# Performance work log

Measured on AMD Instinct MI355X. Metric: run time of the kernel, lower is better.

## Reference

```python
import itertools
import jax, jax.numpy as jnp
import numpy as np

# ---- JPEG constants (match utils.y_table / utils.c_table) ----
_Y_TABLE = np.array([
    [16, 11, 10, 16, 24, 40, 51, 61],
    [12, 12, 14, 19, 26, 58, 60, 55],
    [14, 13, 16, 24, 40, 57, 69, 56],
    [14, 17, 22, 29, 51, 87, 80, 62],
    [18, 22, 37, 56, 68, 109, 103, 77],
    [24, 35, 55, 64, 81, 104, 113, 92],
    [49, 64, 78, 87, 103, 121, 120, 101],
    [72, 92, 95, 98, 112, 100, 103, 99]], dtype=np.float32)
_C_TABLE = np.full((8, 8), 99, dtype=np.float32)
_C_TABLE[:4, :4] = np.array([[17, 18, 24, 47], [18, 21, 26, 66],
                             [24, 26, 56, 99], [47, 66, 99, 99]], dtype=np.float32)

# RGB -> YCbCr matrix (code defines M then uses M.T via tensordot dims=1)
_YCBCR_M = np.array([[0.299, 0.587, 0.114],
                     [-0.168736, -0.331264, 0.5],
                     [0.5, -0.418688, -0.081312]], dtype=np.float32)
_SHIFT = np.array([0.0, 128.0, 128.0], dtype=np.float32)

_cx = np.cos((2 * np.arange(8)[:, None] + 1) * np.arange(8)[None, :] * np.pi / 16)  # [x,u]
_DCT = np.einsum('xu,yv->xyuv', _cx, _cx).astype(np.float32)
_alpha = np.array([1.0 / np.sqrt(2)] + [1.0] * 7)
_DCT_SCALE = (np.outer(_alpha, _alpha) * 0.25).astype(np.float32)

FACTOR = 1.0
K = 8  # block size


def _block_split(x):
    # x: [B, H, W] -> [B, H*W/64, 8, 8]
    B, H, W = x.shape
    x = x.reshape(B, H // K, K, W // K, K)
    x = jnp.transpose(x, (0, 1, 3, 2, 4))
    return x.reshape(B, -1, K, K)


def _dct_8x8(x):
    # x: [B, N, 8, 8]
    x = x - 128.0
    return jnp.asarray(_DCT_SCALE) * jnp.einsum('bnxy,xyuv->bnuv', x, jnp.asarray(_DCT))


def _avg_pool2(x):
    # 2x2 average pooling, stride 2; x: [B, H, W]
    B, H, W = x.shape
    return x.reshape(B, H // 2, 2, W // 2, 2).mean(axis=(2, 4))


def _compress(image):
    # image: [B, 3, H, W] in [0, 1]
    img = jnp.transpose(image * 255.0, (0, 2, 3, 1))  # [B, H, W, 3]
    ycbcr = jnp.einsum('bhwc,cd->bhwd', img, jnp.asarray(_YCBCR_M.T)) + jnp.asarray(_SHIFT)
    y = ycbcr[..., 0]
    cb = _avg_pool2(ycbcr[..., 1])
    cr = _avg_pool2(ycbcr[..., 2])
    y_q = jnp.round(_dct_8x8(_block_split(y)) / (jnp.asarray(_Y_TABLE) * FACTOR))
    cb_q = jnp.round(_dct_8x8(_block_split(cb)) / (jnp.asarray(_C_TABLE) * FACTOR))
    cr_q = jnp.round(_dct_8x8(_block_split(cr)) / (jnp.asarray(_C_TABLE) * FACTOR))
    return y_q, cb_q, cr_q


def setup_inputs() -> dict:
    key = jax.random.key(0)
    image = jax.random.uniform(key, (32, 3, 512, 512), dtype=jnp.float32)
    return {"image": image}


def reference(image):
    return _compress(image)
```

## Files before the change

kernel.cpp:

```cpp
#include <hip/hip_runtime.h>
#include <cmath>


namespace jc {

constexpr double c1 = 0.98078528040323044912618223613424;
constexpr double c2 = 0.92387953251128675612818318939679;
constexpr double c3 = 0.83146961230254523707878837761791;
constexpr double c4 = 0.70710678118654752440084436210485;
constexpr double c5 = 0.55557023301960222474283081394853;
constexpr double c6 = 0.38268343236508977172845998403040;
constexpr double c7 = 0.19509032201612826784828486847702;
constexpr double alpha0 = 0.70710678118654746171979706919384;

struct Tab {
  float t[4096];
  float sc[64];
  float yq[64];
  float cq[64];
  constexpr Tab() : t(), sc(), yq(), cq() {
    const double CX[8][8] = {
      {1.0,  c1,  c2,  c3,  c4,  c5,  c6,  c7},
      {1.0,  c3,  c6, -c7, -c4, -c1, -c2, -c5},
      {1.0,  c5, -c6, -c1, -c4,  c7,  c2,  c3},
      {1.0,  c7, -c2, -c5,  c4,  c3, -c6, -c1},
      {1.0, -c7, -c2,  c5,  c4, -c3, -c6,  c1},
      {1.0, -c5, -c6,  c1, -c4, -c7,  c2, -c3},
      {1.0, -c3,  c6,  c7, -c4,  c1, -c2,  c5},
      {1.0, -c1,  c2, -c3,  c4, -c5,  c6, -c7}};
    for (int i = 0; i < 64; ++i) {
      const int u = i >> 3, v = i & 7;
      for (int j = 0; j < 64; ++j) {
        const int x = j >> 3, y = j & 7;
        t[i * 64 + j] = (float)(CX[x][u] * CX[y][v]);
      }
      const double au = (u == 0) ? alpha0 : 1.0;
      const double av = (v == 0) ? alpha0 : 1.0;
      sc[i] = (float)((au * av) * 0.25);
    }
    const int YT[64] = {
      16, 11, 10, 16, 24, 40, 51, 61,
      12, 12, 14, 19, 26, 58, 60, 55,
      14, 13, 16, 24, 40, 57, 69, 56,
      14, 17, 22, 29, 51, 87, 80, 62,
      18, 22, 37, 56, 68, 109, 103, 77,
      24, 35, 55, 64, 81, 104, 113, 92,
      49, 64, 78, 87, 103, 121, 120, 101,
      72, 92, 95, 98, 112, 100, 103, 99};
    const int CT[64] = {
      17, 18, 24, 47, 99, 99, 99, 99,
      18, 21, 26, 66, 99, 99, 99, 99,
      24, 26, 56, 99, 99, 99, 99, 99,
      47, 66, 99, 99, 99, 99, 99, 99,
      99, 99, 99, 99, 99, 99, 99, 99,
      99, 99, 99, 99, 99, 99, 99, 99,
      99, 99, 99, 99, 99, 99, 99, 99,
      99, 99, 99, 99, 99, 99, 99, 99};
    for (int i = 0; i < 64; ++i) {
      yq[i] = (float)YT[i];
      cq[i] = (float)CT[i];
    }
  }
};

__device__ constexpr Tab TT;

}

__device__ __forceinline__ float madd(float a, float b, float acc) {
  return __fadd_rn(acc, __fmul_rn(a, b));
}

__device__ __forceinline__ float ylum(float R, float G, float B) {
  const float tR = __fmul_rn(R, 255.0f);
  const float tG = __fmul_rn(G, 255.0f);
  const float tB = __fmul_rn(B, 255.0f);
  float a = __fmul_rn(tR, 0.299f);
  a = madd(tG, 0.587f, a);
  a = madd(tB, 0.114f, a);
  return a;
}

__device__ __forceinline__ float chro(float R, float G, float B,
                                      float kR, float kG, float kB) {
  const float tR = __fmul_rn(R, 255.0f);
  const float tG = __fmul_rn(G, 255.0f);
  const float tB = __fmul_rn(B, 255.0f);
  float a = __fmul_rn(tR, kR);
  a = madd(tG, kG, a);
  a = madd(tB, kB, a);
  return __fadd_rn(a, 128.0f);
}

__global__ __launch_bounds__(64) void jpeg_kernel(const float* __restrict__ img,
                                                  float* __restrict__ out) {
  const int wid = blockIdx.x;
  const int ln = threadIdx.x;

  float X[64];
  float* outp;
  const float* qt;

  if (wid < 2048) {
    const int b = wid >> 6;
    const int r = wid & 63;
    const int gby = (r >> 3) * 8 + (ln >> 3);
    const int gbx = (r & 7) * 8 + (ln & 7);
    const float* rp = img + (size_t)b * 786432 + gby * 4096 + gbx * 8;
#pragma unroll
    for (int x = 0; x < 8; ++x) {
      const float4 r0 = *(const float4*)(rp + x * 512);
      const float4 r1 = *(const float4*)(rp + x * 512 + 4);
      const float4 g0 = *(const float4*)(rp + 262144 + x * 512);
      const float4 g1 = *(const float4*)(rp + 262144 + x * 512 + 4);
      const float4 b0 = *(const float4*)(rp + 524288 + x * 512);
      const float4 b1 = *(const float4*)(rp + 524288 + x * 512 + 4);
      X[x * 8 + 0] = __fsub_rn(ylum(r0.x, g0.x, b0.x), 128.0f);
      X[x * 8 + 1] = __fsub_rn(ylum(r0.y, g0.y, b0.y), 128.0f);
      X[x * 8 + 2] = __fsub_rn(ylum(r0.z, g0.z, b0.z), 128.0f);
      X[x * 8 + 3] = __fsub_rn(ylum(r0.w, g0.w, b0.w), 128.0f);
      X[x * 8 + 4] = __fsub_rn(ylum(r1.x, g1.x, b1.x), 128.0f);
      X[x * 8 + 5] = __fsub_rn(ylum(r1.y, g1.y, b1.y), 128.0f);
      X[x * 8 + 6] = __fsub_rn(ylum(r1.z, g1.z, b1.z), 128.0f);
      X[x * 8 + 7] = __fsub_rn(ylum(r1.w, g1.w, b1.w), 128.0f);
    }
    outp = out + ((size_t)(b * 4096 + gby * 64 + gbx) << 6);
    qt = jc::TT.yq;
  } else {
    const int cw = wid - 2048;
    const int b = cw >> 5;
    const int reg = cw & 31;
    const int typ = ln >> 5;
    const int s = ln & 31;
    const int cby = (reg >> 2) * 4 + (s >> 3);
    const int cbx = (reg & 3) * 8 + (s & 7);
    const float* base = img + (size_t)b * 786432 + cby * 8192 + cbx * 16;
    const float kR = typ ? 0.5f       : -0.168736f;
    const float kG = typ ? -0.418688f : -0.331264f;
    const float kB = typ ? -0.081312f : 0.5f;
#pragma unroll
    for (int pr = 0; pr < 8; ++pr) {
      float px[3][2][16];
#pragma unroll
      for (int c = 0; c < 3; ++c) {
#pragma unroll
        for (int rr = 0; rr < 2; ++rr) {
          const float* p0 = base + c * 262144 + pr * 1024 + rr * 512;
#pragma unroll
          for (int q = 0; q < 4; ++q) {
            const float4 v = *(const float4*)(p0 + q * 4);
            px[c][rr][q * 4 + 0] = v.x;
            px[c][rr][q * 4 + 1] = v.y;
            px[c][rr][q * 4 + 2] = v.z;
            px[c][rr][q * 4 + 3] = v.w;
          }
        }
      }
#pragma unroll
      for (int pc = 0; pc < 8; ++pc) {
        const int c0 = 2 * pc, c1 = 2 * pc + 1;
        const float p00 = chro(px[0][0][c0], px[1][0][c0], px[2][0][c0], kR, kG, kB);
        const float p01 = chro(px[0][0][c1], px[1][0][c1], px[2][0][c1], kR, kG, kB);
        const float p10 = chro(px[0][1][c0], px[1][1][c0], px[2][1][c0], kR, kG, kB);
        const float p11 = chro(px[0][1][c1], px[1][1][c1], px[2][1][c1], kR, kG, kB);
        const float ssum = __fadd_rn(__fadd_rn(__fadd_rn(p00, p01), p10), p11);
        const float m = __fmul_rn(ssum, 0.25f);
        X[pr * 8 + pc] = __fsub_rn(m, 128.0f);
      }
    }
    outp = out + 8388608 + (size_t)typ * 2097152 +
           ((size_t)(b * 1024 + cby * 32 + cbx) << 6);
    qt = jc::TT.cq;
  }

  for (int i = 0; i < 64; i += 4) {
    const float* tr = jc::TT.t + i * 64;
    float a0 = 0.0f, a1 = 0.0f, a2 = 0.0f, a3 = 0.0f;
#pragma unroll
    for (int j = 0; j < 64; ++j) {
      a0 = madd(X[j], tr[j], a0);
      a1 = madd(X[j], tr[64 + j], a1);
      a2 = madd(X[j], tr[128 + j], a2);
      a3 = madd(X[j], tr[192 + j], a3);
    }
    float4 stv;
    stv.x = rintf(__fdiv_rn(__fmul_rn(jc::TT.sc[i + 0], a0), qt[i + 0]));
    stv.y = rintf(__fdiv_rn(__fmul_rn(jc::TT.sc[i + 1], a1), qt[i + 1]));
    stv.z = rintf(__fdiv_rn(__fmul_rn(jc::TT.sc[i + 2], a2), qt[i + 2]));
    stv.w = rintf(__fdiv_rn(__fmul_rn(jc::TT.sc[i + 3], a3), qt[i + 3]));
    *(float4*)(outp + i) = stv;
  }
}

extern "C" void kernel_launch(void* const* d_in, const int* in_sizes, int n_in,
                              void* d_out, int out_size, void* d_ws, size_t ws_size,
                              hipStream_t stream) {
  (void)in_sizes; (void)n_in; (void)d_ws; (void)ws_size; (void)out_size;
  const float* img = (const float*)d_in[0];
  float* out = (float*)d_out;
  jpeg_kernel<<<dim3(3072), dim3(64), 0, stream>>>(img, out);
}
```

Measured before the change: 226.6 us.

## Split each block's DCT across four waves via shared-memory staging

Workgroups grow from 64 to 256 threads. Each wave loads a quarter of the pixel rows and writes the color-converted values into a padded shared-memory tile. After a barrier, each wave computes 16 of the 64 DCT coefficients for every block, with the basis row address made wave-uniform through readfirstlane so table values can come from scalar registers. Inline-asm mul/add wrappers keep the arithmetic unfused, replacing __fmul_rn/__fadd_rn. The aim is four times the threads in flight and fewer per-thread registers, at the cost of LDS traffic and a barrier.

```diff
diff --git a/kernel.cpp b/kernel.cpp
--- a/kernel.cpp
+++ b/kernel.cpp
@@ -67,62 +67,73 @@
 
 }
 
-__device__ __forceinline__ float madd(float a, float b, float acc) {
-  return __fadd_rn(acc, __fmul_rn(a, b));
+__device__ __forceinline__ float vmul(float a, float b) {
+  float r; asm("v_mul_f32 %0, %1, %2" : "=v"(r) : "v"(a), "v"(b)); return r;
+}
+__device__ __forceinline__ float vadd(float a, float b) {
+  float r; asm("v_add_f32 %0, %1, %2" : "=v"(r) : "v"(a), "v"(b)); return r;
+}
+__device__ __forceinline__ float vsubf(float a, float b) {
+  float r; asm("v_sub_f32 %0, %1, %2" : "=v"(r) : "v"(a), "v"(b)); return r;
+}
+__device__ __forceinline__ float vmul_sv(float su, float v) {
+  float r; asm("v_mul_f32 %0, %1, %2" : "=v"(r) : "s"(su), "v"(v)); return r;
 }
 
 __device__ __forceinline__ float ylum(float R, float G, float B) {
-  const float tR = __fmul_rn(R, 255.0f);
-  const float tG = __fmul_rn(G, 255.0f);
-  const float tB = __fmul_rn(B, 255.0f);
-  float a = __fmul_rn(tR, 0.299f);
-  a = madd(tG, 0.587f, a);
-  a = madd(tB, 0.114f, a);
+  const float tR = vmul(R, 255.0f);
+  const float tG = vmul(G, 255.0f);
+  const float tB = vmul(B, 255.0f);
+  float a = vmul(tR, 0.299f);
+  a = vadd(a, vmul(tG, 0.587f));
+  a = vadd(a, vmul(tB, 0.114f));
   return a;
 }
 
-__device__ __forceinline__ float chro(float R, float G, float B,
-                                      float kR, float kG, float kB) {
-  const float tR = __fmul_rn(R, 255.0f);
-  const float tG = __fmul_rn(G, 255.0f);
-  const float tB = __fmul_rn(B, 255.0f);
-  float a = __fmul_rn(tR, kR);
-  a = madd(tG, kG, a);
-  a = madd(tB, kB, a);
-  return __fadd_rn(a, 128.0f);
-}
-
-__global__ __launch_bounds__(64) void jpeg_kernel(const float* __restrict__ img,
-                                                  float* __restrict__ out) {
+__device__ __forceinline__ float chro_t(float tR, float tG, float tB,
+                                        float kR, float kG, float kB) {
+  float a = vmul(tR, kR);
+  a = vadd(a, vmul(tG, kG));
+  a = vadd(a, vmul(tB, kB));
+  return vadd(a, 128.0f);
+}
+
+__global__ __launch_bounds__(256, 4) void jpeg_kernel(const float* __restrict__ img,
+                                                      float* __restrict__ out) {
+  __shared__ float Xs[64][65];
+
   const int wid = blockIdx.x;
-  const int ln = threadIdx.x;
-
-  float X[64];
+  const int t = threadIdx.x;
+  const int sub = t & 63;
+  const int iq = t >> 6;
+
   float* outp;
   const float* qt;
 
   if (wid < 2048) {
     const int b = wid >> 6;
     const int r = wid & 63;
-    const int gby = (r >> 3) * 8 + (ln >> 3);
-    const int gbx = (r & 7) * 8 + (ln & 7);
+    const int gby = (r >> 3) * 8 + (sub >> 3);
+    const int gbx = (r & 7) * 8 + (sub & 7);
     const float* rp = img + (size_t)b * 786432 + gby * 4096 + gbx * 8;
 #pragma unroll
-    for (int x = 0; x < 8; ++x) {
+    for (int xr = 0; xr < 2; ++xr) {
+      const int x = iq * 2 + xr;
       const float4 r0 = *(const float4*)(rp + x * 512);
       const float4 r1 = *(const float4*)(rp + x * 512 + 4);
       const float4 g0 = *(const float4*)(rp + 262144 + x * 512);
       const float4 g1 = *(const float4*)(rp + 262144 + x * 512 + 4);
       const float4 b0 = *(const float4*)(rp + 524288 + x * 512);
       const float4 b1 = *(const float4*)(rp + 524288 + x * 512 + 4);
-      X[x * 8 + 0] = __fsub_rn(ylum(r0.x, g0.x, b0.x), 128.0f);
-      X[x * 8 + 1] = __fsub_rn(ylum(r0.y, g0.y, b0.y), 128.0f);
-      X[x * 8 + 2] = __fsub_rn(ylum(r0.z, g0.z, b0.z), 128.0f);
-      X[x * 8 + 3] = __fsub_rn(ylum(r0.w, g0.w, b0.w), 128.0f);
-      X[x * 8 + 4] = __fsub_rn(ylum(r1.x, g1.x, b1.x), 128.0f);
-      X[x * 8 + 5] = __fsub_rn(ylum(r1.y, g1.y, b1.y), 128.0f);
-      X[x * 8 + 6] = __fsub_rn(ylum(r1.z, g1.z, b1.z), 128.0f);
-      X[x * 8 + 7] = __fsub_rn(ylum(r1.w, g1.w, b1.w), 128.0f);
+      float* xp = &Xs[sub][x * 8];
+      xp[0] = vsubf(ylum(r0.x, g0.x, b0.x), 128.0f);
+      xp[1] = vsubf(ylum(r0.y, g0.y, b0.y), 128.0f);
+      xp[2] = vsubf(ylum(r0.z, g0.z, b0.z), 128.0f);
+      xp[3] = vsubf(ylum(r0.w, g0.w, b0.w), 128.0f);
+      xp[4] = vsubf(ylum(r1.x, g1.x, b1.x), 128.0f);
+      xp[5] = vsubf(ylum(r1.y, g1.y, b1.y), 128.0f);
+      xp[6] = vsubf(ylum(r1.z, g1.z, b1.z), 128.0f);
+      xp[7] = vsubf(ylum(r1.w, g1.w, b1.w), 128.0f);
     }
     outp = out + ((size_t)(b * 4096 + gby * 64 + gbx) << 6);
     qt = jc::TT.yq;
@@ -130,65 +141,92 @@
     const int cw = wid - 2048;
     const int b = cw >> 5;
     const int reg = cw & 31;
-    const int typ = ln >> 5;
-    const int s = ln & 31;
-    const int cby = (reg >> 2) * 4 + (s >> 3);
-    const int cbx = (reg & 3) * 8 + (s & 7);
-    const float* base = img + (size_t)b * 786432 + cby * 8192 + cbx * 16;
-    const float kR = typ ? 0.5f       : -0.168736f;
-    const float kG = typ ? -0.418688f : -0.331264f;
-    const float kB = typ ? -0.081312f : 0.5f;
-#pragma unroll
-    for (int pr = 0; pr < 8; ++pr) {
+    {
+      const int p = t & 31;
+      const int rr = t >> 5;
+      const int cby = (reg >> 2) * 4 + (p >> 3);
+      const int cbx = (reg & 3) * 8 + (p & 7);
+      const float* base = img + (size_t)b * 786432 + cby * 8192 + cbx * 16 + rr * 1024;
       float px[3][2][16];
 #pragma unroll
       for (int c = 0; c < 3; ++c) {
 #pragma unroll
-        for (int rr = 0; rr < 2; ++rr) {
-          const float* p0 = base + c * 262144 + pr * 1024 + rr * 512;
+        for (int rw = 0; rw < 2; ++rw) {
+          const float* p0 = base + c * 262144 + rw * 512;
 #pragma unroll
           for (int q = 0; q < 4; ++q) {
             const float4 v = *(const float4*)(p0 + q * 4);
-            px[c][rr][q * 4 + 0] = v.x;
-            px[c][rr][q * 4 + 1] = v.y;
-            px[c][rr][q * 4 + 2] = v.z;
-            px[c][rr][q * 4 + 3] = v.w;
+            px[c][rw][q * 4 + 0] = v.x;
+            px[c][rw][q * 4 + 1] = v.y;
+            px[c][rw][q * 4 + 2] = v.z;
+            px[c][rw][q * 4 + 3] = v.w;
           }
         }
       }
 #pragma unroll
       for (int pc = 0; pc < 8; ++pc) {
-        const int c0 = 2 * pc, c1 = 2 * pc + 1;
-        const float p00 = chro(px[0][0][c0], px[1][0][c0], px[2][0][c0], kR, kG, kB);
-        const float p01 = chro(px[0][0][c1], px[1][0][c1], px[2][0][c1], kR, kG, kB);
-        const float p10 = chro(px[0][1][c0], px[1][1][c0], px[2][1][c0], kR, kG, kB);
-        const float p11 = chro(px[0][1][c1], px[1][1][c1], px[2][1][c1], kR, kG, kB);
-        const float ssum = __fadd_rn(__fadd_rn(__fadd_rn(p00, p01), p10), p11);
-        const float m = __fmul_rn(ssum, 0.25f);
-        X[pr * 8 + pc] = __fsub_rn(m, 128.0f);
+#pragma unroll
+        for (int typ = 0; typ < 2; ++typ) {
+          const float kR = typ ? 0.5f       : -0.168736f;
+          const float kG = typ ? -0.418688f : -0.331264f;
+          const float kB = typ ? -0.081312f : 0.5f;
+          float pv[4];
+#pragma unroll
+          for (int q = 0; q < 4; ++q) {
+            const int rw = q >> 1;
+            const int cc = 2 * pc + (q & 1);
+            const float tR = vmul(px[0][rw][cc], 255.0f);
+            const float tG = vmul(px[1][rw][cc], 255.0f);
+            const float tB = vmul(px[2][rw][cc], 255.0f);
+            pv[q] = chro_t(tR, tG, tB, kR, kG, kB);
+          }
+          const float ssum = vadd(vadd(vadd(pv[0], pv[1]), pv[2]), pv[3]);
+          const float m = vmul(ssum, 0.25f);
+          Xs[typ * 32 + p][rr * 8 + pc] = vsubf(m, 128.0f);
+        }
       }
     }
+    const int typ = sub >> 5;
+    const int pp = sub & 31;
+    const int cby = (reg >> 2) * 4 + (pp >> 3);
+    const int cbx = (reg & 3) * 8 + (pp & 7);
     outp = out + 8388608 + (size_t)typ * 2097152 +
            ((size_t)(b * 1024 + cby * 32 + cbx) << 6);
     qt = jc::TT.cq;
   }
 
-  for (int i = 0; i < 64; i += 4) {
-    const float* tr = jc::TT.t + i * 64;
-    float a0 = 0.0f, a1 = 0.0f, a2 = 0.0f, a3 = 0.0f;
-#pragma unroll
-    for (int j = 0; j < 64; ++j) {
-      a0 = madd(X[j], tr[j], a0);
-      a1 = madd(X[j], tr[64 + j], a1);
-      a2 = madd(X[j], tr[128 + j], a2);
-      a3 = madd(X[j], tr[192 + j], a3);
-    }
+  __syncthreads();
+
+  const int ibase = __builtin_amdgcn_readfirstlane(iq) * 16;
+  const float* __restrict__ xrow = Xs[sub];
+  const float* tr = jc::TT.t + ibase * 64;
+
+  float acc[16];
+#pragma unroll
+  for (int k = 0; k < 16; ++k) acc[k] = 0.0f;
+
+#pragma unroll
+  for (int j = 0; j < 64; ++j) {
+    const float xv = xrow[j];
+#pragma unroll
+    for (int k = 0; k < 16; ++k) {
+      acc[k] = vadd(acc[k], vmul_sv(tr[k * 64 + j], xv));
+    }
+  }
+
+  float* op = outp + ibase;
+#pragma unroll
+  for (int k4 = 0; k4 < 4; ++k4) {
     float4 stv;
-    stv.x = rintf(__fdiv_rn(__fmul_rn(jc::TT.sc[i + 0], a0), qt[i + 0]));
-    stv.y = rintf(__fdiv_rn(__fmul_rn(jc::TT.sc[i + 1], a1), qt[i + 1]));
-    stv.z = rintf(__fdiv_rn(__fmul_rn(jc::TT.sc[i + 2], a2), qt[i + 2]));
-    stv.w = rintf(__fdiv_rn(__fmul_rn(jc::TT.sc[i + 3], a3), qt[i + 3]));
-    *(float4*)(outp + i) = stv;
+    stv.x = rintf(__fdiv_rn(vmul_sv(jc::TT.sc[ibase + k4 * 4 + 0], acc[k4 * 4 + 0]),
+                            qt[ibase + k4 * 4 + 0]));
+    stv.y = rintf(__fdiv_rn(vmul_sv(jc::TT.sc[ibase + k4 * 4 + 1], acc[k4 * 4 + 1]),
+                            qt[ibase + k4 * 4 + 1]));
+    stv.z = rintf(__fdiv_rn(vmul_sv(jc::TT.sc[ibase + k4 * 4 + 2], acc[k4 * 4 + 2]),
+                            qt[ibase + k4 * 4 + 2]));
+    stv.w = rintf(__fdiv_rn(vmul_sv(jc::TT.sc[ibase + k4 * 4 + 3], acc[k4 * 4 + 3]),
+                            qt[ibase + k4 * 4 + 3]));
+    *(float4*)(op + k4 * 4) = stv;
   }
 }
 
@@ -198,5 +236,5 @@
   (void)in_sizes; (void)n_in; (void)d_ws; (void)ws_size; (void)out_size;
   const float* img = (const float*)d_in[0];
   float* out = (float*)d_out;
-  jpeg_kernel<<<dim3(3072), dim3(64), 0, stream>>>(img, out);
-}
+  jpeg_kernel<<<dim3(3072), dim3(256), 0, stream>>>(img, out);
+}
```

After: 276.2 us. 21.9% more time.
